# Optimization experiments

Hardware: AMD Instinct MI355X
Metric: run time of the kernel (lower is better)

## Reference

```python
import jax, jax.numpy as jnp
import numpy as np

B, S, H, I, SI, E, TOPK = 2, 1024, 1024, 512, 2048, 8, 2


def setup_inputs() -> dict:
    key = jax.random.key(0)
    ks = jax.random.split(key, 8)
    w = 0.02
    return {
        "hidden_states": jax.random.normal(ks[0], (B, S, H), jnp.float32),
        "router_weight": jax.random.normal(ks[1], (E, H), jnp.float32) * w,
        "gate_up_proj": jax.random.normal(ks[2], (E, 2 * I, H), jnp.float32) * w,
        "down_proj": jax.random.normal(ks[3], (E, H, I), jnp.float32) * w,
        "shared_gate_w": jax.random.normal(ks[4], (SI, H), jnp.float32) * w,
        "shared_up_w": jax.random.normal(ks[5], (SI, H), jnp.float32) * w,
        "shared_down_w": jax.random.normal(ks[6], (H, SI), jnp.float32) * w,
        "shared_expert_gate_w": jax.random.normal(ks[7], (1, H), jnp.float32) * w,
    }


def reference(hidden_states, router_weight, gate_up_proj, down_proj,
              shared_gate_w, shared_up_w, shared_down_w, shared_expert_gate_w):
    b, s, h = hidden_states.shape
    x = hidden_states.reshape(-1, h)  # [T, H]

    # shared expert (SwiGLU)
    shared = (jax.nn.silu(x @ shared_gate_w.T) * (x @ shared_up_w.T)) @ shared_down_w.T  # [T, H]

    # top-k softmax router (softmax in fp32, renormalized top-k weights)
    logits = x @ router_weight.T  # [T, E]
    probs = jax.nn.softmax(logits.astype(jnp.float32), axis=-1)
    top_v, top_i = jax.lax.top_k(probs, TOPK)
    top_v = (top_v / jnp.sum(top_v, axis=-1, keepdims=True)).astype(logits.dtype)  # [T, K]

    # combine weights per (token, expert): sum over k of routing weight * one_hot
    cw = jnp.sum(jax.nn.one_hot(top_i, E, dtype=top_v.dtype) * top_v[..., None], axis=1)  # [T, E]

    # grouped-expert SwiGLU (dense compute, masked combine == gather/scatter math)
    gu = jnp.einsum('th,eih->eti', x, gate_up_proj)  # [E, T, 2I]
    gate, up = jnp.split(gu, 2, axis=-1)
    act = jax.nn.silu(gate) * up  # [E, T, I]
    per_expert = jnp.einsum('eti,ehi->eth', act, down_proj)  # [E, T, H]
    expert_out = jnp.einsum('eth,te->th', per_expert, cw)  # [T, H]

    out = expert_out + jax.nn.sigmoid(x @ shared_expert_gate_w.T) * shared
    return out.reshape(b, s, h)
```

## Files before the change

kernel.cpp:

```cpp
#include <hip/hip_runtime.h>

#define T_TOK 2048
#define H_DIM 1024
#define I_DIM 512
#define SI_DIM 2048
#define E_NUM 8
#define NSLOT 4096

typedef __attribute__((ext_vector_type(8))) short short8;
typedef __attribute__((ext_vector_type(4))) float floatx4;

__device__ inline unsigned short f2bf(float f) {
  unsigned u = __builtin_bit_cast(unsigned, f);
  u = (u + 0x7FFFu + ((u >> 16) & 1u)) >> 16;
  return (unsigned short)u;
}
__device__ inline float bf2f(unsigned short u) {
  return __builtin_bit_cast(float, (unsigned)u << 16);
}

__device__ inline void gl_lds16(const void* g, void* l) {
  __builtin_amdgcn_global_load_lds(
      (const __attribute__((address_space(1))) unsigned int*)g,
      (__attribute__((address_space(3))) unsigned int*)l, 16, 0, 0);
}

__global__ __launch_bounds__(256) void cast_router(
    const float* __restrict__ x, const float* __restrict__ rw,
    const float* __restrict__ segw,
    const float* __restrict__ s1, const float* __restrict__ s2,
    const float* __restrict__ s3, const float* __restrict__ s4,
    const float* __restrict__ s5,
    unsigned short* __restrict__ d0, unsigned short* __restrict__ d1,
    unsigned short* __restrict__ d2, unsigned short* __restrict__ d3,
    unsigned short* __restrict__ d4, unsigned short* __restrict__ d5,
    int* __restrict__ top2, float2* __restrict__ w01, float* __restrict__ sg) {
  const int bid = blockIdx.x;
  if (bid < 512) {
    int t = bid * 4 + (threadIdx.x >> 6);
    int lane = threadIdx.x & 63;
    const float* xt = x + (long)t * H_DIM;
    float xv[16];
#pragma unroll
    for (int j = 0; j < 16; ++j) xv[j] = xt[j * 64 + lane];
    float dots[9];
#pragma unroll
    for (int e = 0; e < 8; ++e) {
      const float* w = rw + e * H_DIM;
      float s = 0.f;
#pragma unroll
      for (int j = 0; j < 16; ++j) s += xv[j] * w[j * 64 + lane];
      dots[e] = s;
    }
    {
      float s = 0.f;
#pragma unroll
      for (int j = 0; j < 16; ++j) s += xv[j] * segw[j * 64 + lane];
      dots[8] = s;
    }
#pragma unroll
    for (int off = 32; off > 0; off >>= 1) {
#pragma unroll
      for (int e = 0; e < 9; ++e) dots[e] += __shfl_xor(dots[e], off, 64);
    }
    if (lane == 0) {
      int e0 = 0;
      for (int e = 1; e < 8; ++e)
        if (dots[e] > dots[e0]) e0 = e;
      int e1 = (e0 == 0) ? 1 : 0;
      for (int e = 0; e < 8; ++e)
        if (e != e0 && dots[e] > dots[e1]) e1 = e;
      float p1 = expf(dots[e1] - dots[e0]);
      top2[t] = e0 | (e1 << 8);
      w01[t] = make_float2(1.f / (1.f + p1), p1 / (1.f + p1));
      sg[t] = 1.f / (1.f + expf(-dots[8]));
    }
  } else {
    long g = (long)(bid - 512) * 256 + threadIdx.x;
    const float* s;
    unsigned short* d;
    long off;
    if (g < 262144L)        { s = x;  d = d0; off = g; }
    else if (g < 1310720L)  { s = s1; d = d1; off = g - 262144L; }
    else if (g < 1835008L)  { s = s2; d = d2; off = g - 1310720L; }
    else if (g < 2097152L)  { s = s3; d = d3; off = g - 1835008L; }
    else if (g < 2359296L)  { s = s4; d = d4; off = g - 2097152L; }
    else                    { s = s5; d = d5; off = g - 2359296L; }
    const float4* sp = (const float4*)s;
    float4 v0 = sp[off * 2];
    float4 v1 = sp[off * 2 + 1];
    uint4 u;
    u.x = (unsigned)f2bf(v0.x) | ((unsigned)f2bf(v0.y) << 16);
    u.y = (unsigned)f2bf(v0.z) | ((unsigned)f2bf(v0.w) << 16);
    u.z = (unsigned)f2bf(v1.x) | ((unsigned)f2bf(v1.y) << 16);
    u.w = (unsigned)f2bf(v1.z) | ((unsigned)f2bf(v1.w) << 16);
    ((uint4*)d)[off] = u;
  }
}

__global__ __launch_bounds__(256) void build_lists(
    const int* __restrict__ top2, int* __restrict__ cnt, int* __restrict__ ebase,
    int* __restrict__ slot_token, int* __restrict__ tok_slot) {
  const int e = blockIdx.x;
  const int tid = threadIdx.x;
  const int lane = tid & 63, wid = tid >> 6;
  __shared__ int wsum[4], wbelow[4];
  const int base_t = tid * 8;
  int mk[8], kk[8];
  int c = 0, below = 0;
#pragma unroll
  for (int j = 0; j < 8; ++j) {
    int p = top2[base_t + j];
    int e0 = p & 0xFF, e1 = (p >> 8) & 0xFF;
    below += (e0 < e) + (e1 < e);
    int m = 0, k = 0;
    if (e0 == e) { m = 1; k = 0; }
    else if (e1 == e) { m = 1; k = 1; }
    mk[j] = m; kk[j] = k;
    c += m;
  }
  int inc = c;
#pragma unroll
  for (int off = 1; off < 64; off <<= 1) {
    int n = __shfl_up(inc, off, 64);
    if (lane >= off) inc += n;
  }
  int bsum = below;
#pragma unroll
  for (int off = 32; off > 0; off >>= 1) bsum += __shfl_xor(bsum, off, 64);
  if (lane == 63) wsum[wid] = inc;
  if (lane == 0) wbelow[wid] = bsum;
  __syncthreads();
  int woff = 0;
#pragma unroll
  for (int i = 0; i < 4; ++i)
    if (i < wid) woff += wsum[i];
  int baseE = wbelow[0] + wbelow[1] + wbelow[2] + wbelow[3];
  int pos = baseE + woff + inc - c;
#pragma unroll
  for (int j = 0; j < 8; ++j) {
    if (mk[j]) {
      slot_token[pos] = base_t + j;
      tok_slot[2 * (base_t + j) + kk[j]] = pos;
      pos++;
    }
  }
  if (tid == 255) cnt[e] = woff + inc;
  if (tid == 0) ebase[e] = baseE;
}

template <bool GATHER>
__device__ __forceinline__ void swiglu_body(
    char* smem, int bx, int by, int e,
    const unsigned short* __restrict__ A, const unsigned short* __restrict__ Bg,
    const unsigned short* __restrict__ Bu, unsigned short* __restrict__ Out,
    const int* __restrict__ slot_token, const int* __restrict__ cnt,
    const int* __restrict__ ebase, int N, int K, long estrideB) {
  constexpr int BM = 128, BN = 128, BK = 32;
  constexpr int ATILE = BM * BK;
  constexpr int BTILE = BN * BK;
  const int tid = threadIdx.x;
  const int lane = tid & 63;
  const int wid = tid >> 6;
  const int wm = wid & 1;
  const int wn = wid >> 1;
  const int m0 = by * BM;
  const int n0 = bx * BN;
  int Meff = 0, baseE = 0;
  if (GATHER) {
    Meff = cnt[e];
    if (m0 >= Meff) return;
    baseE = ebase[e];
  }
  const unsigned short* BgE = Bg + (long)e * estrideB;
  const unsigned short* BuE = Bu + (long)e * estrideB;

  unsigned short* As = (unsigned short*)smem;
  unsigned short* Bgs = As + 2 * ATILE;
  unsigned short* Bus = Bgs + 2 * BTILE;

  const int lrow = lane >> 2;
  const int lcol = (((lane & 3) ^ ((lrow >> 1) & 3)) << 4);

  const char* aP[2];
  const char* bgP[2];
  const char* buP[2];
#pragma unroll
  for (int i = 0; i < 2; ++i) {
    int m = m0 + wid * 32 + i * 16 + lrow;
    long row;
    if (GATHER) {
      int mm = (m < Meff - 1) ? m : (Meff - 1);
      row = slot_token[baseE + mm];
    } else {
      row = m;
    }
    aP[i] = (const char*)A + row * (long)(K * 2) + lcol;
    int n = n0 + wid * 32 + i * 16 + lrow;
    bgP[i] = (const char*)BgE + (long)n * (K * 2) + lcol;
    buP[i] = (const char*)BuE + (long)n * (K * 2) + lcol;
  }

  floatx4 accG[4][4], accU[4][4];
  floatx4 zero = {0.f, 0.f, 0.f, 0.f};
#pragma unroll
  for (int i = 0; i < 4; ++i)
#pragma unroll
    for (int j = 0; j < 4; ++j) { accG[i][j] = zero; accU[i][j] = zero; }

  const int ar = lane & 15;
  const int aksw = (((lane >> 4) ^ ((ar >> 1) & 3)) << 3);

  auto stage = [&](int p, int k0) {
#pragma unroll
    for (int i = 0; i < 2; ++i) {
      gl_lds16(aP[i] + (long)k0 * 2, &As[p * ATILE + (wid * 32 + i * 16) * BK]);
      gl_lds16(bgP[i] + (long)k0 * 2, &Bgs[p * BTILE + (wid * 32 + i * 16) * BK]);
      gl_lds16(buP[i] + (long)k0 * 2, &Bus[p * BTILE + (wid * 32 + i * 16) * BK]);
    }
  };

  stage(0, 0);
  const int NI = K / BK;
  for (int i = 0; i < NI; ++i) {
    __syncthreads();
    if (i + 1 < NI) stage((i + 1) & 1, (i + 1) * BK);
    const unsigned short* Ab = &As[(i & 1) * ATILE];
    const unsigned short* Gb = &Bgs[(i & 1) * BTILE];
    const unsigned short* Ub = &Bus[(i & 1) * BTILE];
    short8 af[4], bgf[4], buf2[4];
#pragma unroll
    for (int tm = 0; tm < 4; ++tm)
      af[tm] = *(const short8*)&Ab[(wm * 64 + tm * 16 + ar) * BK + aksw];
#pragma unroll
    for (int tn = 0; tn < 4; ++tn) {
      bgf[tn] = *(const short8*)&Gb[(wn * 64 + tn * 16 + ar) * BK + aksw];
      buf2[tn] = *(const short8*)&Ub[(wn * 64 + tn * 16 + ar) * BK + aksw];
    }
#pragma unroll
    for (int tm = 0; tm < 4; ++tm)
#pragma unroll
      for (int tn = 0; tn < 4; ++tn) {
        accG[tm][tn] = __builtin_amdgcn_mfma_f32_16x16x32_bf16(af[tm], bgf[tn], accG[tm][tn], 0, 0, 0);
        accU[tm][tn] = __builtin_amdgcn_mfma_f32_16x16x32_bf16(af[tm], buf2[tn], accU[tm][tn], 0, 0, 0);
      }
  }

#pragma unroll
  for (int tm = 0; tm < 4; ++tm)
#pragma unroll
    for (int tn = 0; tn < 4; ++tn)
#pragma unroll
      for (int r = 0; r < 4; ++r) {
        int row = m0 + wm * 64 + tm * 16 + (lane >> 4) * 4 + r;
        int col = n0 + wn * 64 + tn * 16 + (lane & 15);
        if (!GATHER || row < Meff) {
          float g = accG[tm][tn][r];
          float u = accU[tm][tn][r];
          float act = g / (1.f + expf(-g)) * u;
          Out[(long)(baseE + row) * N + col] = f2bf(act);
        }
      }
}

__global__ __launch_bounds__(256, 2) void swiglu_fused(
    const unsigned short* __restrict__ xb, const unsigned short* __restrict__ sgate,
    const unsigned short* __restrict__ sup, unsigned short* __restrict__ act_s,
    const unsigned short* __restrict__ gup, unsigned short* __restrict__ act_e,
    const int* __restrict__ slot_token, const int* __restrict__ cnt,
    const int* __restrict__ ebase) {
  __shared__ __align__(16) char smem[49152];
  int bid = blockIdx.x;
  if (bid < 256) {
    swiglu_body<false>(smem, bid & 15, bid >> 4, 0, xb, sgate, sup, act_s,
                       nullptr, nullptr, nullptr, SI_DIM, H_DIM, 0);
  } else {
    int b2 = bid - 256;
    int e = b2 >> 6;
    int rem = b2 & 63;
    swiglu_body<true>(smem, rem & 3, rem >> 2, e, xb, gup,
                      gup + (long)I_DIM * H_DIM, act_e, slot_token, cnt,
                      ebase, I_DIM, H_DIM, (long)2 * I_DIM * H_DIM);
  }
}

template <int MODE>
__device__ __forceinline__ void down_body(
    char* smem, int bx, int by, int e,
    const unsigned short* __restrict__ A, const unsigned short* __restrict__ B,
    float* __restrict__ OutF, unsigned short* __restrict__ OutB,
    const int* __restrict__ ebase, const int* __restrict__ cnt,
    int N, int Kstride, int kbeg, int kcnt, long estrideB) {
  constexpr int BM = 128, BN = 256, BK = 32;
  constexpr int ATILE = BM * BK;
  constexpr int BTILE = BN * BK;
  const int tid = threadIdx.x;
  const int lane = tid & 63;
  const int wid = tid >> 6;
  const int wm = wid & 1;
  const int wn = wid >> 1;
  const int m0 = by * BM;
  const int n0 = bx * BN;
  int Meff = 0, baseE = 0;
  if (MODE == 1) {
    Meff = cnt[e];
    if (m0 >= Meff) return;
    baseE = ebase[e];
  }
  const unsigned short* BE = B + (long)e * estrideB;

  unsigned short* As = (unsigned short*)smem;
  unsigned short* Bs = As + 2 * ATILE;

  const int lrow = lane >> 2;
  const int lcol = (((lane & 3) ^ ((lrow >> 1) & 3)) << 4);

  const char* aP[2];
  const char* bP[4];
#pragma unroll
  for (int i = 0; i < 2; ++i) {
    int m = m0 + wid * 32 + i * 16 + lrow;
    long arow;
    if (MODE == 1) {
      int mm = (m < Meff - 1) ? m : (Meff - 1);
      arow = baseE + mm;
    } else {
      arow = m;
    }
    aP[i] = (const char*)A + arow * (long)(Kstride * 2) + (long)kbeg * 2 + lcol;
  }
#pragma unroll
  for (int i = 0; i < 4; ++i) {
    int n = n0 + wid * 64 + i * 16 + lrow;
    bP[i] = (const char*)BE + (long)n * (Kstride * 2) + (long)kbeg * 2 + lcol;
  }

  floatx4 acc[4][8];
  floatx4 zero = {0.f, 0.f, 0.f, 0.f};
#pragma unroll
  for (int i = 0; i < 4; ++i)
#pragma unroll
    for (int j = 0; j < 8; ++j) acc[i][j] = zero;

  const int ar = lane & 15;
  const int aksw = (((lane >> 4) ^ ((ar >> 1) & 3)) << 3);

  auto stage = [&](int p, int k0) {
#pragma unroll
    for (int i = 0; i < 2; ++i)
      gl_lds16(aP[i] + (long)k0 * 2, &As[p * ATILE + (wid * 32 + i * 16) * BK]);
#pragma unroll
    for (int i = 0; i < 4; ++i)
      gl_lds16(bP[i] + (long)k0 * 2, &Bs[p * BTILE + (wid * 64 + i * 16) * BK]);
  };

  stage(0, 0);
  const int NI = kcnt / BK;
  for (int i = 0; i < NI; ++i) {
    __syncthreads();
    if (i + 1 < NI) stage((i + 1) & 1, (i + 1) * BK);
    const unsigned short* Ab = &As[(i & 1) * ATILE];
    const unsigned short* Bb = &Bs[(i & 1) * BTILE];
    short8 af[4], bf[8];
#pragma unroll
    for (int tm = 0; tm < 4; ++tm)
      af[tm] = *(const short8*)&Ab[(wm * 64 + tm * 16 + ar) * BK + aksw];
#pragma unroll
    for (int tn = 0; tn < 8; ++tn)
      bf[tn] = *(const short8*)&Bb[(wn * 128 + tn * 16 + ar) * BK + aksw];
#pragma unroll
    for (int tm = 0; tm < 4; ++tm)
#pragma unroll
      for (int tn = 0; tn < 8; ++tn)
        acc[tm][tn] = __builtin_amdgcn_mfma_f32_16x16x32_bf16(af[tm], bf[tn], acc[tm][tn], 0, 0, 0);
  }

#pragma unroll
  for (int tm = 0; tm < 4; ++tm)
#pragma unroll
    for (int r = 0; r < 4; ++r) {
      int row = m0 + wm * 64 + tm * 16 + (lane >> 4) * 4 + r;
#pragma unroll
      for (int tn = 0; tn < 8; ++tn) {
        int col = n0 + wn * 128 + tn * 16 + (lane & 15);
        float v = acc[tm][tn][r];
        if (MODE == 0) {
          OutF[(long)row * N + col] = v;
        } else if (MODE == 2) {
          OutB[(long)row * N + col] = f2bf(v);
        } else if (row < Meff) {
          OutB[(long)(baseE + row) * N + col] = f2bf(v);
        }
      }
    }
}

__global__ __launch_bounds__(256, 2) void down_fused(
    const unsigned short* __restrict__ act_s, const unsigned short* __restrict__ sdown,
    float* __restrict__ out, unsigned short* __restrict__ spart,
    const unsigned short* __restrict__ act_e, const unsigned short* __restrict__ downw,
    unsigned short* __restrict__ eout, const int* __restrict__ ebase,
    const int* __restrict__ cnt) {
  __shared__ __align__(16) char smem[49152];
  int bid = blockIdx.x;
  if (bid < 128) {
    int ks = bid >> 6;
    int rem = bid & 63;
    if (ks == 0)
      down_body<0>(smem, rem & 3, rem >> 2, 0, act_s, sdown, out, nullptr,
                   nullptr, nullptr, H_DIM, SI_DIM, 0, 1024, 0);
    else
      down_body<2>(smem, rem & 3, rem >> 2, 0, act_s, sdown, nullptr, spart,
                   nullptr, nullptr, H_DIM, SI_DIM, 1024, 1024, 0);
  } else {
    int b2 = bid - 128;
    int e = b2 >> 6;
    int rem = b2 & 63;
    down_body<1>(smem, rem & 3, rem >> 2, e, act_e, downw, nullptr, eout,
                 ebase, cnt, H_DIM, I_DIM, 0, I_DIM, (long)H_DIM * I_DIM);
  }
}

__global__ __launch_bounds__(256) void combine_kernel(
    float* __restrict__ out, const unsigned short* __restrict__ spart,
    const unsigned short* __restrict__ eout, const float* __restrict__ sg,
    const float2* __restrict__ w01, const int* __restrict__ tok_slot) {
  int t = blockIdx.x;
  int c = threadIdx.x;
  float sgr = sg[t];
  float2 wr = w01[t];
  int s0 = tok_slot[2 * t];
  int s1 = tok_slot[2 * t + 1];
  ushort4 p1 = ((const ushort4*)(spart + (long)t * H_DIM))[c];
  ushort4 e0 = ((const ushort4*)(eout + (long)s0 * H_DIM))[c];
  ushort4 e1 = ((const ushort4*)(eout + (long)s1 * H_DIM))[c];
  float4* op = &((float4*)(out + (long)t * H_DIM))[c];
  float4 o = *op;
  o.x = sgr * (o.x + bf2f(p1.x)) + wr.x * bf2f(e0.x) + wr.y * bf2f(e1.x);
  o.y = sgr * (o.y + bf2f(p1.y)) + wr.x * bf2f(e0.y) + wr.y * bf2f(e1.y);
  o.z = sgr * (o.z + bf2f(p1.z)) + wr.x * bf2f(e0.z) + wr.y * bf2f(e1.z);
  o.w = sgr * (o.w + bf2f(p1.w)) + wr.x * bf2f(e0.w) + wr.y * bf2f(e1.w);
  *op = o;
}

extern "C" void kernel_launch(void* const* d_in, const int* in_sizes, int n_in,
                              void* d_out, int out_size, void* d_ws, size_t ws_size,
                              hipStream_t stream) {
  const float* x = (const float*)d_in[0];
  const float* rw = (const float*)d_in[1];
  const float* gup = (const float*)d_in[2];
  const float* dwn = (const float*)d_in[3];
  const float* sgw = (const float*)d_in[4];
  const float* suw = (const float*)d_in[5];
  const float* sdw = (const float*)d_in[6];
  const float* segw = (const float*)d_in[7];
  float* out = (float*)d_out;

  char* w = (char*)d_ws;
  unsigned short* xb = (unsigned short*)(w + 0);
  unsigned short* gup_b = (unsigned short*)(w + 4194304L);
  unsigned short* down_b = (unsigned short*)(w + 20971520L);
  unsigned short* sgate_b = (unsigned short*)(w + 29360128L);
  unsigned short* sup_b = (unsigned short*)(w + 33554432L);
  unsigned short* sdown_b = (unsigned short*)(w + 37748736L);
  unsigned short* act_s = (unsigned short*)(w + 41943040L);
  unsigned short* act_e = (unsigned short*)(w + 50331648L);
  unsigned short* eout = (unsigned short*)(w + 54525952L);
  float* sg = (float*)(w + 62914560L);
  int* top2 = (int*)(w + 62922752L);
  float2* w01 = (float2*)(w + 62930944L);
  int* cnt = (int*)(w + 62947328L);
  int* ebase = (int*)(w + 62947584L);
  int* slot_token = (int*)(w + 62947840L);
  int* tok_slot = (int*)(w + 62964224L);
  unsigned short* spart = xb;

  cast_router<<<10752, 256, 0, stream>>>(x, rw, segw, gup, dwn, sgw, suw, sdw,
                                         xb, gup_b, down_b, sgate_b, sup_b,
                                         sdown_b, top2, w01, sg);
  build_lists<<<E_NUM, 256, 0, stream>>>(top2, cnt, ebase, slot_token, tok_slot);
  swiglu_fused<<<768, 256, 0, stream>>>(xb, sgate_b, sup_b, act_s, gup_b,
                                        act_e, slot_token, cnt, ebase);
  down_fused<<<640, 256, 0, stream>>>(act_s, sdown_b, out, spart, act_e,
                                      down_b, eout, ebase, cnt);
  combine_kernel<<<T_TOK, 256, 0, stream>>>(out, spart, eout, sg, w01, tok_slot);
}
```

Baseline: 197.5 us.

## Triple-buffer LDS staging with explicit vmcnt waits in GEMM mainloops

Both the SwiGLU and down-projection GEMM bodies move from double to triple buffering of shared-memory tiles. Loads run two stages ahead. Each iteration waits with a partial s_waitcnt vmcnt and a raw s_barrier instead of a full __syncthreads. The next-next stage is issued after the LDS fragment reads, so global-to-LDS loads overlap more compute. LDS per block grows from 48KB to 72KB, which may limit occupancy to fewer blocks per CU than the launch bound of 2 suggests.

```diff
diff --git a/kernel.cpp b/kernel.cpp
--- a/kernel.cpp
+++ b/kernel.cpp
@@ -176,8 +176,8 @@
   const unsigned short* BuE = Bu + (long)e * estrideB;
 
   unsigned short* As = (unsigned short*)smem;
-  unsigned short* Bgs = As + 2 * ATILE;
-  unsigned short* Bus = Bgs + 2 * BTILE;
+  unsigned short* Bgs = As + 3 * ATILE;
+  unsigned short* Bus = Bgs + 3 * BTILE;
 
   const int lrow = lane >> 2;
   const int lcol = (((lane & 3) ^ ((lrow >> 1) & 3)) << 4);
@@ -221,13 +221,21 @@
   };
 
   stage(0, 0);
+  stage(1, BK);
   const int NI = K / BK;
+  int cur = 0;
   for (int i = 0; i < NI; ++i) {
-    __syncthreads();
-    if (i + 1 < NI) stage((i + 1) & 1, (i + 1) * BK);
-    const unsigned short* Ab = &As[(i & 1) * ATILE];
-    const unsigned short* Gb = &Bgs[(i & 1) * BTILE];
-    const unsigned short* Ub = &Bus[(i & 1) * BTILE];
+    if (i + 1 < NI) {
+      asm volatile("s_waitcnt vmcnt(6)" ::: "memory");
+    } else {
+      asm volatile("s_waitcnt vmcnt(0)" ::: "memory");
+    }
+    __builtin_amdgcn_sched_barrier(0);
+    __builtin_amdgcn_s_barrier();
+    __builtin_amdgcn_sched_barrier(0);
+    const unsigned short* Ab = &As[cur * ATILE];
+    const unsigned short* Gb = &Bgs[cur * BTILE];
+    const unsigned short* Ub = &Bus[cur * BTILE];
     short8 af[4], bgf[4], buf2[4];
 #pragma unroll
     for (int tm = 0; tm < 4; ++tm)
@@ -236,6 +244,11 @@
     for (int tn = 0; tn < 4; ++tn) {
       bgf[tn] = *(const short8*)&Gb[(wn * 64 + tn * 16 + ar) * BK + aksw];
       buf2[tn] = *(const short8*)&Ub[(wn * 64 + tn * 16 + ar) * BK + aksw];
+    }
+    if (i + 2 < NI) {
+      int stg = cur + 2;
+      if (stg >= 3) stg -= 3;
+      stage(stg, (i + 2) * BK);
     }
 #pragma unroll
     for (int tm = 0; tm < 4; ++tm)
@@ -244,6 +257,7 @@
         accG[tm][tn] = __builtin_amdgcn_mfma_f32_16x16x32_bf16(af[tm], bgf[tn], accG[tm][tn], 0, 0, 0);
         accU[tm][tn] = __builtin_amdgcn_mfma_f32_16x16x32_bf16(af[tm], buf2[tn], accU[tm][tn], 0, 0, 0);
       }
+    cur = (cur + 1 == 3) ? 0 : cur + 1;
   }
 
 #pragma unroll
@@ -269,7 +283,7 @@
     const unsigned short* __restrict__ gup, unsigned short* __restrict__ act_e,
     const int* __restrict__ slot_token, const int* __restrict__ cnt,
     const int* __restrict__ ebase) {
-  __shared__ __align__(16) char smem[49152];
+  __shared__ __align__(16) char smem[73728];
   int bid = blockIdx.x;
   if (bid < 256) {
     swiglu_body<false>(smem, bid & 15, bid >> 4, 0, xb, sgate, sup, act_s,
@@ -310,7 +324,7 @@
   const unsigned short* BE = B + (long)e * estrideB;
 
   unsigned short* As = (unsigned short*)smem;
-  unsigned short* Bs = As + 2 * ATILE;
+  unsigned short* Bs = As + 3 * ATILE;
 
   const int lrow = lane >> 2;
   const int lcol = (((lane & 3) ^ ((lrow >> 1) & 3)) << 4);
@@ -355,12 +369,20 @@
   };
 
   stage(0, 0);
+  stage(1, BK);
   const int NI = kcnt / BK;
+  int cur = 0;
   for (int i = 0; i < NI; ++i) {
-    __syncthreads();
-    if (i + 1 < NI) stage((i + 1) & 1, (i + 1) * BK);
-    const unsigned short* Ab = &As[(i & 1) * ATILE];
-    const unsigned short* Bb = &Bs[(i & 1) * BTILE];
+    if (i + 1 < NI) {
+      asm volatile("s_waitcnt vmcnt(6)" ::: "memory");
+    } else {
+      asm volatile("s_waitcnt vmcnt(0)" ::: "memory");
+    }
+    __builtin_amdgcn_sched_barrier(0);
+    __builtin_amdgcn_s_barrier();
+    __builtin_amdgcn_sched_barrier(0);
+    const unsigned short* Ab = &As[cur * ATILE];
+    const unsigned short* Bb = &Bs[cur * BTILE];
     short8 af[4], bf[8];
 #pragma unroll
     for (int tm = 0; tm < 4; ++tm)
@@ -368,11 +390,17 @@
 #pragma unroll
     for (int tn = 0; tn < 8; ++tn)
       bf[tn] = *(const short8*)&Bb[(wn * 128 + tn * 16 + ar) * BK + aksw];
+    if (i + 2 < NI) {
+      int stg = cur + 2;
+      if (stg >= 3) stg -= 3;
+      stage(stg, (i + 2) * BK);
+    }
 #pragma unroll
     for (int tm = 0; tm < 4; ++tm)
 #pragma unroll
       for (int tn = 0; tn < 8; ++tn)
         acc[tm][tn] = __builtin_amdgcn_mfma_f32_16x16x32_bf16(af[tm], bf[tn], acc[tm][tn], 0, 0, 0);
+    cur = (cur + 1 == 3) ? 0 : cur + 1;
   }
 
 #pragma unroll
@@ -401,7 +429,7 @@
     const unsigned short* __restrict__ act_e, const unsigned short* __restrict__ downw,
     unsigned short* __restrict__ eout, const int* __restrict__ ebase,
     const int* __restrict__ cnt) {
-  __shared__ __align__(16) char smem[49152];
+  __shared__ __align__(16) char smem[73728];
   int bid = blockIdx.x;
   if (bid < 128) {
     int ks = bid >> 6;
```

Result: no change. 199.2 us (+0.9%).

## Load fp32 weights directly into LDS and convert to bf16 inside GEMMs

Applied to the files above, without the earlier changes.

The separate pre-pass that casts all weight matrices to bf16 is removed. The GEMM kernels now stage fp32 weight tiles into LDS with a swizzled layout and convert them to bf16 fragments with v_cvt_pk_bf16_f32 before the MFMA. This removes a full write and re-read of the bf16 weight copies. In exchange it doubles the weight bytes moved per GEMM tile, enlarges LDS use to 80KB per block, and adds conversion instructions inside the inner loop.

```diff
diff --git a/kernel.cpp b/kernel.cpp
--- a/kernel.cpp
+++ b/kernel.cpp
@@ -25,15 +25,21 @@
       (__attribute__((address_space(3))) unsigned int*)l, 16, 0, 0);
 }
 
+__device__ __forceinline__ short8 bfrag_f32(const float* Bb, int rr, int kk) {
+  float4 a0 = *(const float4*)&Bb[rr * 32 + (((2 * kk) ^ (rr & 7)) << 2)];
+  float4 a1 = *(const float4*)&Bb[rr * 32 + (((2 * kk + 1) ^ (rr & 7)) << 2)];
+  unsigned u0, u1, u2, u3;
+  asm("v_cvt_pk_bf16_f32 %0, %1, %2" : "=v"(u0) : "v"(a0.x), "v"(a0.y));
+  asm("v_cvt_pk_bf16_f32 %0, %1, %2" : "=v"(u1) : "v"(a0.z), "v"(a0.w));
+  asm("v_cvt_pk_bf16_f32 %0, %1, %2" : "=v"(u2) : "v"(a1.x), "v"(a1.y));
+  asm("v_cvt_pk_bf16_f32 %0, %1, %2" : "=v"(u3) : "v"(a1.z), "v"(a1.w));
+  uint4 r = make_uint4(u0, u1, u2, u3);
+  return __builtin_bit_cast(short8, r);
+}
+
 __global__ __launch_bounds__(256) void cast_router(
     const float* __restrict__ x, const float* __restrict__ rw,
-    const float* __restrict__ segw,
-    const float* __restrict__ s1, const float* __restrict__ s2,
-    const float* __restrict__ s3, const float* __restrict__ s4,
-    const float* __restrict__ s5,
-    unsigned short* __restrict__ d0, unsigned short* __restrict__ d1,
-    unsigned short* __restrict__ d2, unsigned short* __restrict__ d3,
-    unsigned short* __restrict__ d4, unsigned short* __restrict__ d5,
+    const float* __restrict__ segw, unsigned short* __restrict__ xb,
     int* __restrict__ top2, float2* __restrict__ w01, float* __restrict__ sg) {
   const int bid = blockIdx.x;
   if (bid < 512) {
@@ -77,24 +83,15 @@
     }
   } else {
     long g = (long)(bid - 512) * 256 + threadIdx.x;
-    const float* s;
-    unsigned short* d;
-    long off;
-    if (g < 262144L)        { s = x;  d = d0; off = g; }
-    else if (g < 1310720L)  { s = s1; d = d1; off = g - 262144L; }
-    else if (g < 1835008L)  { s = s2; d = d2; off = g - 1310720L; }
-    else if (g < 2097152L)  { s = s3; d = d3; off = g - 1835008L; }
-    else if (g < 2359296L)  { s = s4; d = d4; off = g - 2097152L; }
-    else                    { s = s5; d = d5; off = g - 2359296L; }
-    const float4* sp = (const float4*)s;
-    float4 v0 = sp[off * 2];
-    float4 v1 = sp[off * 2 + 1];
+    const float4* sp = (const float4*)x;
+    float4 v0 = sp[g * 2];
+    float4 v1 = sp[g * 2 + 1];
     uint4 u;
     u.x = (unsigned)f2bf(v0.x) | ((unsigned)f2bf(v0.y) << 16);
     u.y = (unsigned)f2bf(v0.z) | ((unsigned)f2bf(v0.w) << 16);
     u.z = (unsigned)f2bf(v1.x) | ((unsigned)f2bf(v1.y) << 16);
     u.w = (unsigned)f2bf(v1.z) | ((unsigned)f2bf(v1.w) << 16);
-    ((uint4*)d)[off] = u;
+    ((uint4*)xb)[g] = u;
   }
 }
 
@@ -152,13 +149,13 @@
 template <bool GATHER>
 __device__ __forceinline__ void swiglu_body(
     char* smem, int bx, int by, int e,
-    const unsigned short* __restrict__ A, const unsigned short* __restrict__ Bg,
-    const unsigned short* __restrict__ Bu, unsigned short* __restrict__ Out,
+    const unsigned short* __restrict__ A, const float* __restrict__ Bg,
+    const float* __restrict__ Bu, unsigned short* __restrict__ Out,
     const int* __restrict__ slot_token, const int* __restrict__ cnt,
     const int* __restrict__ ebase, int N, int K, long estrideB) {
   constexpr int BM = 128, BN = 128, BK = 32;
   constexpr int ATILE = BM * BK;
-  constexpr int BTILE = BN * BK;
+  constexpr int BTILEF = BN * BK;
   const int tid = threadIdx.x;
   const int lane = tid & 63;
   const int wid = tid >> 6;
@@ -172,19 +169,17 @@
     if (m0 >= Meff) return;
     baseE = ebase[e];
   }
-  const unsigned short* BgE = Bg + (long)e * estrideB;
-  const unsigned short* BuE = Bu + (long)e * estrideB;
+  const float* BgE = Bg + (long)e * estrideB;
+  const float* BuE = Bu + (long)e * estrideB;
 
   unsigned short* As = (unsigned short*)smem;
-  unsigned short* Bgs = As + 2 * ATILE;
-  unsigned short* Bus = Bgs + 2 * BTILE;
+  float* BgsF = (float*)(smem + 16384);
+  float* BusF = (float*)(smem + 49152);
 
   const int lrow = lane >> 2;
   const int lcol = (((lane & 3) ^ ((lrow >> 1) & 3)) << 4);
 
   const char* aP[2];
-  const char* bgP[2];
-  const char* buP[2];
 #pragma unroll
   for (int i = 0; i < 2; ++i) {
     int m = m0 + wid * 32 + i * 16 + lrow;
@@ -196,9 +191,17 @@
       row = m;
     }
     aP[i] = (const char*)A + row * (long)(K * 2) + lcol;
-    int n = n0 + wid * 32 + i * 16 + lrow;
-    bgP[i] = (const char*)BgE + (long)n * (K * 2) + lcol;
-    buP[i] = (const char*)BuE + (long)n * (K * 2) + lcol;
+  }
+
+  const int br8 = lane >> 3;
+  const int bck = (lane & 7) ^ (br8 & 7);
+  const char* bgPf[4];
+  const char* buPf[4];
+#pragma unroll
+  for (int i = 0; i < 4; ++i) {
+    int n = n0 + wid * 32 + i * 8 + br8;
+    bgPf[i] = (const char*)BgE + (long)n * (K * 4) + bck * 16;
+    buPf[i] = (const char*)BuE + (long)n * (K * 4) + bck * 16;
   }
 
   floatx4 accG[4][4], accU[4][4];
@@ -210,13 +213,16 @@
 
   const int ar = lane & 15;
   const int aksw = (((lane >> 4) ^ ((ar >> 1) & 3)) << 3);
+  const int kk = lane >> 4;
 
   auto stage = [&](int p, int k0) {
 #pragma unroll
-    for (int i = 0; i < 2; ++i) {
+    for (int i = 0; i < 2; ++i)
       gl_lds16(aP[i] + (long)k0 * 2, &As[p * ATILE + (wid * 32 + i * 16) * BK]);
-      gl_lds16(bgP[i] + (long)k0 * 2, &Bgs[p * BTILE + (wid * 32 + i * 16) * BK]);
-      gl_lds16(buP[i] + (long)k0 * 2, &Bus[p * BTILE + (wid * 32 + i * 16) * BK]);
+#pragma unroll
+    for (int i = 0; i < 4; ++i) {
+      gl_lds16(bgPf[i] + (long)k0 * 4, &BgsF[p * BTILEF + (wid * 32 + i * 8) * BK]);
+      gl_lds16(buPf[i] + (long)k0 * 4, &BusF[p * BTILEF + (wid * 32 + i * 8) * BK]);
     }
   };
 
@@ -226,16 +232,17 @@
     __syncthreads();
     if (i + 1 < NI) stage((i + 1) & 1, (i + 1) * BK);
     const unsigned short* Ab = &As[(i & 1) * ATILE];
-    const unsigned short* Gb = &Bgs[(i & 1) * BTILE];
-    const unsigned short* Ub = &Bus[(i & 1) * BTILE];
+    const float* Gb = &BgsF[(i & 1) * BTILEF];
+    const float* Ub = &BusF[(i & 1) * BTILEF];
     short8 af[4], bgf[4], buf2[4];
 #pragma unroll
     for (int tm = 0; tm < 4; ++tm)
       af[tm] = *(const short8*)&Ab[(wm * 64 + tm * 16 + ar) * BK + aksw];
 #pragma unroll
     for (int tn = 0; tn < 4; ++tn) {
-      bgf[tn] = *(const short8*)&Gb[(wn * 64 + tn * 16 + ar) * BK + aksw];
-      buf2[tn] = *(const short8*)&Ub[(wn * 64 + tn * 16 + ar) * BK + aksw];
+      int rr = wn * 64 + tn * 16 + ar;
+      bgf[tn] = bfrag_f32(Gb, rr, kk);
+      buf2[tn] = bfrag_f32(Ub, rr, kk);
     }
 #pragma unroll
     for (int tm = 0; tm < 4; ++tm)
@@ -264,15 +271,15 @@
 }
 
 __global__ __launch_bounds__(256, 2) void swiglu_fused(
-    const unsigned short* __restrict__ xb, const unsigned short* __restrict__ sgate,
-    const unsigned short* __restrict__ sup, unsigned short* __restrict__ act_s,
-    const unsigned short* __restrict__ gup, unsigned short* __restrict__ act_e,
+    const unsigned short* __restrict__ xb, const float* __restrict__ sgw,
+    const float* __restrict__ suw, unsigned short* __restrict__ act_s,
+    const float* __restrict__ gup, unsigned short* __restrict__ act_e,
     const int* __restrict__ slot_token, const int* __restrict__ cnt,
     const int* __restrict__ ebase) {
-  __shared__ __align__(16) char smem[49152];
+  __shared__ __align__(16) char smem[81920];
   int bid = blockIdx.x;
   if (bid < 256) {
-    swiglu_body<false>(smem, bid & 15, bid >> 4, 0, xb, sgate, sup, act_s,
+    swiglu_body<false>(smem, bid & 15, bid >> 4, 0, xb, sgw, suw, act_s,
                        nullptr, nullptr, nullptr, SI_DIM, H_DIM, 0);
   } else {
     int b2 = bid - 256;
@@ -287,13 +294,13 @@
 template <int MODE>
 __device__ __forceinline__ void down_body(
     char* smem, int bx, int by, int e,
-    const unsigned short* __restrict__ A, const unsigned short* __restrict__ B,
+    const unsigned short* __restrict__ A, const float* __restrict__ B,
     float* __restrict__ OutF, unsigned short* __restrict__ OutB,
     const int* __restrict__ ebase, const int* __restrict__ cnt,
     int N, int Kstride, int kbeg, int kcnt, long estrideB) {
   constexpr int BM = 128, BN = 256, BK = 32;
   constexpr int ATILE = BM * BK;
-  constexpr int BTILE = BN * BK;
+  constexpr int BTILEF = BN * BK;
   const int tid = threadIdx.x;
   const int lane = tid & 63;
   const int wid = tid >> 6;
@@ -307,16 +314,15 @@
     if (m0 >= Meff) return;
     baseE = ebase[e];
   }
-  const unsigned short* BE = B + (long)e * estrideB;
+  const float* BE = B + (long)e * estrideB;
 
   unsigned short* As = (unsigned short*)smem;
-  unsigned short* Bs = As + 2 * ATILE;
+  float* BsF = (float*)(smem + 16384);
 
   const int lrow = lane >> 2;
   const int lcol = (((lane & 3) ^ ((lrow >> 1) & 3)) << 4);
 
   const char* aP[2];
-  const char* bP[4];
 #pragma unroll
   for (int i = 0; i < 2; ++i) {
     int m = m0 + wid * 32 + i * 16 + lrow;
@@ -329,10 +335,14 @@
     }
     aP[i] = (const char*)A + arow * (long)(Kstride * 2) + (long)kbeg * 2 + lcol;
   }
-#pragma unroll
-  for (int i = 0; i < 4; ++i) {
-    int n = n0 + wid * 64 + i * 16 + lrow;
-    bP[i] = (const char*)BE + (long)n * (Kstride * 2) + (long)kbeg * 2 + lcol;
+
+  const int br8 = lane >> 3;
+  const int bck = (lane & 7) ^ (br8 & 7);
+  const char* bPf[8];
+#pragma unroll
+  for (int i = 0; i < 8; ++i) {
+    int n = n0 + wid * 64 + i * 8 + br8;
+    bPf[i] = (const char*)BE + (long)n * (Kstride * 4) + (long)kbeg * 4 + bck * 16;
   }
 
   floatx4 acc[4][8];
@@ -344,14 +354,15 @@
 
   const int ar = lane & 15;
   const int aksw = (((lane >> 4) ^ ((ar >> 1) & 3)) << 3);
+  const int kk = lane >> 4;
 
   auto stage = [&](int p, int k0) {
 #pragma unroll
     for (int i = 0; i < 2; ++i)
       gl_lds16(aP[i] + (long)k0 * 2, &As[p * ATILE + (wid * 32 + i * 16) * BK]);
 #pragma unroll
-    for (int i = 0; i < 4; ++i)
-      gl_lds16(bP[i] + (long)k0 * 2, &Bs[p * BTILE + (wid * 64 + i * 16) * BK]);
+    for (int i = 0; i < 8; ++i)
+      gl_lds16(bPf[i] + (long)k0 * 4, &BsF[p * BTILEF + (wid * 64 + i * 8) * BK]);
   };
 
   stage(0, 0);
@@ -360,14 +371,14 @@
     __syncthreads();
     if (i + 1 < NI) stage((i + 1) & 1, (i + 1) * BK);
     const unsigned short* Ab = &As[(i & 1) * ATILE];
-    const unsigned short* Bb = &Bs[(i & 1) * BTILE];
+    const float* Bb = &BsF[(i & 1) * BTILEF];
     short8 af[4], bf[8];
 #pragma unroll
     for (int tm = 0; tm < 4; ++tm)
       af[tm] = *(const short8*)&Ab[(wm * 64 + tm * 16 + ar) * BK + aksw];
 #pragma unroll
     for (int tn = 0; tn < 8; ++tn)
-      bf[tn] = *(const short8*)&Bb[(wn * 128 + tn * 16 + ar) * BK + aksw];
+      bf[tn] = bfrag_f32(Bb, wn * 128 + tn * 16 + ar, kk);
 #pragma unroll
     for (int tm = 0; tm < 4; ++tm)
 #pragma unroll
@@ -380,43 +391,43 @@
 #pragma unroll
     for (int r = 0; r < 4; ++r) {
       int row = m0 + wm * 64 + tm * 16 + (lane >> 4) * 4 + r;
+      if (MODE == 1 && row >= Meff) continue;
+      long orow = (MODE == 1) ? (long)(baseE + row) : (long)row;
 #pragma unroll
       for (int tn = 0; tn < 8; ++tn) {
         int col = n0 + wn * 128 + tn * 16 + (lane & 15);
         float v = acc[tm][tn][r];
         if (MODE == 0) {
-          OutF[(long)row * N + col] = v;
-        } else if (MODE == 2) {
-          OutB[(long)row * N + col] = f2bf(v);
-        } else if (row < Meff) {
-          OutB[(long)(baseE + row) * N + col] = f2bf(v);
+          OutF[orow * N + col] = v;
+        } else {
+          OutB[orow * N + col] = f2bf(v);
         }
       }
     }
 }
 
 __global__ __launch_bounds__(256, 2) void down_fused(
-    const unsigned short* __restrict__ act_s, const unsigned short* __restrict__ sdown,
+    const unsigned short* __restrict__ act_s, const float* __restrict__ sdw,
     float* __restrict__ out, unsigned short* __restrict__ spart,
-    const unsigned short* __restrict__ act_e, const unsigned short* __restrict__ downw,
+    const unsigned short* __restrict__ act_e, const float* __restrict__ dwn,
     unsigned short* __restrict__ eout, const int* __restrict__ ebase,
     const int* __restrict__ cnt) {
-  __shared__ __align__(16) char smem[49152];
+  __shared__ __align__(16) char smem[81920];
   int bid = blockIdx.x;
   if (bid < 128) {
     int ks = bid >> 6;
     int rem = bid & 63;
     if (ks == 0)
-      down_body<0>(smem, rem & 3, rem >> 2, 0, act_s, sdown, out, nullptr,
+      down_body<0>(smem, rem & 3, rem >> 2, 0, act_s, sdw, out, nullptr,
                    nullptr, nullptr, H_DIM, SI_DIM, 0, 1024, 0);
     else
-      down_body<2>(smem, rem & 3, rem >> 2, 0, act_s, sdown, nullptr, spart,
+      down_body<2>(smem, rem & 3, rem >> 2, 0, act_s, sdw, nullptr, spart,
                    nullptr, nullptr, H_DIM, SI_DIM, 1024, 1024, 0);
   } else {
     int b2 = bid - 128;
     int e = b2 >> 6;
     int rem = b2 & 63;
-    down_body<1>(smem, rem & 3, rem >> 2, e, act_e, downw, nullptr, eout,
+    down_body<1>(smem, rem & 3, rem >> 2, e, act_e, dwn, nullptr, eout,
                  ebase, cnt, H_DIM, I_DIM, 0, I_DIM, (long)H_DIM * I_DIM);
   }
 }
@@ -458,30 +469,23 @@
 
   char* w = (char*)d_ws;
   unsigned short* xb = (unsigned short*)(w + 0);
-  unsigned short* gup_b = (unsigned short*)(w + 4194304L);
-  unsigned short* down_b = (unsigned short*)(w + 20971520L);
-  unsigned short* sgate_b = (unsigned short*)(w + 29360128L);
-  unsigned short* sup_b = (unsigned short*)(w + 33554432L);
-  unsigned short* sdown_b = (unsigned short*)(w + 37748736L);
-  unsigned short* act_s = (unsigned short*)(w + 41943040L);
-  unsigned short* act_e = (unsigned short*)(w + 50331648L);
-  unsigned short* eout = (unsigned short*)(w + 54525952L);
-  float* sg = (float*)(w + 62914560L);
-  int* top2 = (int*)(w + 62922752L);
-  float2* w01 = (float2*)(w + 62930944L);
-  int* cnt = (int*)(w + 62947328L);
-  int* ebase = (int*)(w + 62947584L);
-  int* slot_token = (int*)(w + 62947840L);
-  int* tok_slot = (int*)(w + 62964224L);
+  unsigned short* act_s = (unsigned short*)(w + 4194304L);
+  unsigned short* act_e = (unsigned short*)(w + 12582912L);
+  unsigned short* eout = (unsigned short*)(w + 16777216L);
+  float* sg = (float*)(w + 25165824L);
+  int* top2 = (int*)(w + 25174016L);
+  float2* w01 = (float2*)(w + 25182208L);
+  int* cnt = (int*)(w + 25198592L);
+  int* ebase = (int*)(w + 25198848L);
+  int* slot_token = (int*)(w + 25199104L);
+  int* tok_slot = (int*)(w + 25215488L);
   unsigned short* spart = xb;
 
-  cast_router<<<10752, 256, 0, stream>>>(x, rw, segw, gup, dwn, sgw, suw, sdw,
-                                         xb, gup_b, down_b, sgate_b, sup_b,
-                                         sdown_b, top2, w01, sg);
+  cast_router<<<1536, 256, 0, stream>>>(x, rw, segw, xb, top2, w01, sg);
   build_lists<<<E_NUM, 256, 0, stream>>>(top2, cnt, ebase, slot_token, tok_slot);
-  swiglu_fused<<<768, 256, 0, stream>>>(xb, sgate_b, sup_b, act_s, gup_b,
-                                        act_e, slot_token, cnt, ebase);
-  down_fused<<<640, 256, 0, stream>>>(act_s, sdown_b, out, spart, act_e,
-                                      down_b, eout, ebase, cnt);
+  swiglu_fused<<<768, 256, 0, stream>>>(xb, sgw, suw, act_s, gup, act_e,
+                                        slot_token, cnt, ebase);
+  down_fused<<<640, 256, 0, stream>>>(act_s, sdw, out, spart, act_e, dwn,
+                                      eout, ebase, cnt);
   combine_kernel<<<T_TOK, 256, 0, stream>>>(out, spart, eout, sg, w01, tok_slot);
 }
```

Measured after the change: 207.7 us. 1.05x slower.
